# Optimization experiments

Hardware: AMD Instinct MI355X
Metric: run time of the kernel (lower is better)

The kernel has to match this reference:

```python
import jax, jax.numpy as jnp
import numpy as np

B = 16384          # batch
NS = 26            # sparse features
ND = 13            # dense features
V = 100000         # vocab per sparse feature
E = 16             # embedding size
H = 400            # dnn hidden
DNN_IN = NS * E + ND  # 429


def setup_inputs() -> dict:
    key = jax.random.key(0)
    ks = jax.random.split(key, 12)
    X_sparse = jax.random.randint(ks[0], (B, NS), 0, V, dtype=jnp.int32)
    X_dense = jax.random.normal(ks[1], (B, ND), dtype=jnp.float32)
    # stacked per-feature embedding tables: [NS, V, dim]
    emb1 = jax.random.normal(ks[2], (NS, V, 1), dtype=jnp.float32) * 1e-4
    emb2 = jax.random.normal(ks[3], (NS, V, E), dtype=jnp.float32) * 1e-4
    lin_weight = jax.random.normal(ks[4], (ND, 1), dtype=jnp.float32) * 1e-4
    bias = jnp.zeros((1,), dtype=jnp.float32)
    W0 = jax.random.normal(ks[5], (DNN_IN, H), dtype=jnp.float32) * 1e-4
    b0 = jnp.zeros((H,), dtype=jnp.float32)
    W1 = jax.random.normal(ks[6], (H, H), dtype=jnp.float32) * 1e-4
    b1 = jnp.zeros((H,), dtype=jnp.float32)
    W2 = jax.random.normal(ks[7], (H, H), dtype=jnp.float32) * 1e-4
    b2 = jnp.zeros((H,), dtype=jnp.float32)
    W_out = jax.random.normal(ks[8], (H, 1), dtype=jnp.float32) * 1e-4
    return {"X_sparse": X_sparse, "X_dense": X_dense, "emb1": emb1, "emb2": emb2,
            "lin_weight": lin_weight, "bias": bias, "W0": W0, "b0": b0,
            "W1": W1, "b1": b1, "W2": W2, "b2": b2, "W_out": W_out}


def reference(X_sparse, X_dense, emb1, emb2, lin_weight, bias, W0, b0, W1, b1, W2, b2, W_out):
    fidx = jnp.arange(NS)[None, :]            # [1, NS] feature indices
    # ---- FM linear term ----
    e1 = emb1[fidx, X_sparse][..., 0]          # [B, NS] per-feature scalar embeddings
    linear_sparse = jnp.sum(e1, axis=-1, keepdims=True)            # [B, 1]
    linear_dense = X_dense @ lin_weight                            # [B, 1]
    logit = linear_sparse + linear_dense
    # ---- FM second-order cross term ----
    e2 = emb2[fidx, X_sparse]                  # [B, NS, E]
    square_of_sum = jnp.square(jnp.sum(e2, axis=1))                # [B, E]
    sum_of_square = jnp.sum(jnp.square(e2), axis=1)                # [B, E]
    cross = 0.5 * jnp.sum(square_of_sum - sum_of_square, axis=-1, keepdims=True)
    logit = logit + cross
    # ---- DNN (dropout p=0 -> identity) ----
    dnn_in = jnp.concatenate([e2.reshape(e2.shape[0], -1), X_dense], axis=-1)  # [B, 429]
    h = jax.nn.relu(dnn_in @ W0 + b0)
    h = jax.nn.relu(h @ W1 + b1)
    h = jax.nn.relu(h @ W2 + b2)
    logit = logit + h @ W_out
    return logit + bias
```

## Files before the change

kernel.cpp:

```cpp
#include <hip/hip_runtime.h>
#include <hip/hip_bf16.h>

#define B_     16384
#define NS_    26
#define ND_    13
#define V_     100000
#define H_     400
#define NP     448
#define MT     64
#define ASTR   456
#define WCHB   (448 * 64)
#define WQTR   (112 * 64)

#define ACT_OFF   0
#define WBUF_OFF  (MT * ASTR)
#define FMV_OFF   (WBUF_OFF + 2 * WCHB)
#define DOT_OFF   (FMV_OFF + 256)
#define LDSB      (DOT_OFF + 256)

#define WAIT_VM7  0x0F77
#define WAIT_VM0  0x0F70

#define SC_A1   2097152.0f
#define SC_A2   2147483648.0f
#define SC_F0   0.125f
#define SC_F1   0.25f
#define SC_G    1.1368683772161603e-13f

typedef float f32x4 __attribute__((ext_vector_type(4)));

__device__ __forceinline__ unsigned char f2fp8(float v) {
  int pk = __builtin_amdgcn_cvt_pk_fp8_f32(v, v, 0, false);
  return (unsigned char)(pk & 0xff);
}

__global__ __launch_bounds__(256) void prep_w(
    const float* __restrict__ W0, const float* __restrict__ W1,
    const float* __restrict__ W2, const float* __restrict__ b0,
    const float* __restrict__ b1, const float* __restrict__ b2,
    const float* __restrict__ Wout,
    unsigned char* __restrict__ W0t, unsigned char* __restrict__ W1t,
    unsigned char* __restrict__ W2t, float* __restrict__ b0p,
    float* __restrict__ b1p, float* __restrict__ b2p,
    float* __restrict__ woutp) {
  const int blk = blockIdx.x;
  const int tid = threadIdx.x;
  if (blk < 147) {
    const int layer = blk / 49;
    const int t = blk - layer * 49;
    const int k0 = (t / 7) * 64, n0 = (t - (t / 7) * 7) * 64;
    const float* W = (layer == 0) ? W0 : (layer == 1) ? W1 : W2;
    unsigned char* Wt = (layer == 0) ? W0t : (layer == 1) ? W1t : W2t;
    const int Kdim = (layer == 0) ? 429 : 400;
    __shared__ float tile[64][65];
#pragma unroll
    for (int p = 0; p < 16; ++p) {
      int kk = p * 4 + (tid >> 6);
      int k = k0 + kk;
      int n = n0 + (tid & 63);
      float v = (k < Kdim && n < H_) ? W[k * H_ + n] : 0.f;
      tile[kk][tid & 63] = v;
    }
    __syncthreads();
#pragma unroll
    for (int p = 0; p < 4; ++p) {
      int nn = p * 16 + (tid >> 4);
      int n = n0 + nn;
      int k4 = (tid & 15) * 4;
      float sc[4];
#pragma unroll
      for (int i = 0; i < 4; ++i) {
        int kabs = k0 + k4 + i;
        sc[i] = (layer == 0 && kabs >= 416) ? 262144.0f : 4096.0f;
      }
      float v0 = tile[k4 + 0][nn] * sc[0];
      float v1 = tile[k4 + 1][nn] * sc[1];
      float v2 = tile[k4 + 2][nn] * sc[2];
      float v3 = tile[k4 + 3][nn] * sc[3];
      int w = __builtin_amdgcn_cvt_pk_fp8_f32(v0, v1, 0, false);
      w = __builtin_amdgcn_cvt_pk_fp8_f32(v2, v3, w, true);
      *(unsigned int*)(Wt + (size_t)n * NP + k0 + k4) = (unsigned int)w;
    }
  } else {
    for (int it = 0; it < 7; ++it) {
      int j = it * 256 + tid;
      if (j < NP)              b0p[j]          = (j < H_) ? b0[j] * SC_A1 : 0.f;
      else if (j < 2 * NP)     b1p[j - NP]     = (j - NP < H_) ? b1[j - NP] * SC_A2 : 0.f;
      else if (j < 3 * NP)     b2p[j - 2*NP]   = (j - 2*NP < H_) ? b2[j - 2*NP] : 0.f;
      else if (j < 4 * NP)     woutp[j - 3*NP] = (j - 3*NP < H_) ? Wout[j - 3*NP] : 0.f;
    }
  }
}

__device__ __forceinline__ void stage_w_chunk(
    const unsigned char* __restrict__ Wt, int kt, unsigned char* wb,
    int wave, int lane) {
  const unsigned char* wrow = Wt + (size_t)(wave * 112) * NP + kt * 64;
  unsigned char* lbase = wb + wave * WQTR;
#pragma unroll
  for (int i = 0; i < 7; ++i) {
    int s = i * 64 + lane;
    int nl = s >> 2;
    int g = (s & 3) ^ ((nl >> 1) & 3);
    const unsigned char* gp = wrow + (size_t)nl * NP + g * 16;
    unsigned char* lp = lbase + (size_t)(i * 64) * 16;
    __builtin_amdgcn_global_load_lds(
        (const __attribute__((address_space(1))) unsigned int*)gp,
        (__attribute__((address_space(3))) unsigned int*)lp, 16, 0, 0);
  }
}

__global__ __launch_bounds__(256, 1) void fused_all(
    const int* __restrict__ Xs, const float* __restrict__ Xd,
    const float* __restrict__ emb1, const float* __restrict__ emb2,
    const float* __restrict__ linw, const float* __restrict__ bias,
    const unsigned char* __restrict__ W0t, const unsigned char* __restrict__ W1t,
    const unsigned char* __restrict__ W2t,
    const float* __restrict__ b0p, const float* __restrict__ b1p,
    const float* __restrict__ b2p, const float* __restrict__ woutp,
    float* __restrict__ out) {
  extern __shared__ char smem[];
  unsigned char* act  = (unsigned char*)(smem + ACT_OFF);
  unsigned char* wbuf = (unsigned char*)(smem + WBUF_OFF);
  float* fmv  = (float*)(smem + FMV_OFF);
  float* dotv = (float*)(smem + DOT_OFF);

  const int tid  = threadIdx.x;
  const int wave = tid >> 6;
  const int lane = tid & 63;
  const int quad = lane >> 4;
  const int l16  = lane & 15;
  const int r0   = blockIdx.x * MT;

  stage_w_chunk(W0t, 0, wbuf, wave, lane);

  {
    if (tid < 64) dotv[tid] = 0.f;
    const int r   = lane >> 2;
    const int t4  = lane & 3;
    const int row = wave * 16 + r;
    const int gr  = r0 + row;
    const int* xs = Xs + gr * NS_;

    f32x4 sum = {0.f, 0.f, 0.f, 0.f}, sq = {0.f, 0.f, 0.f, 0.f};
#pragma unroll
    for (int f = 0; f < NS_; ++f) {
      int idx = xs[f];
      f32x4 v = *(const f32x4*)(emb2 + ((size_t)f * V_ + idx) * 16 + t4 * 4);
      sum += v;
      sq  += v * v;
      int pk = __builtin_amdgcn_cvt_pk_fp8_f32(v[0] * 4096.f, v[1] * 4096.f, 0, false);
      pk = __builtin_amdgcn_cvt_pk_fp8_f32(v[2] * 4096.f, v[3] * 4096.f, pk, true);
      *(unsigned int*)(act + row * ASTR + f * 16 + t4 * 4) = (unsigned int)pk;
    }

    float lin = 0.f;
    for (int f = t4; f < NS_; f += 4)
      lin += emb1[(size_t)f * V_ + xs[f]];

    for (int e = 416 + t4; e < NP; e += 4) act[row * ASTR + e] = 0;
    for (int e = t4; e < ND_; e += 4) {
      float xd = Xd[gr * ND_ + e];
      lin += xd * linw[e];
      act[row * ASTR + 416 + e] = f2fp8(xd * 64.f);
    }

    f32x4 c4 = sum * sum - sq;
    float fm = 0.5f * (c4[0] + c4[1] + c4[2] + c4[3]) + lin;
    fm += __shfl_xor(fm, 1, 64);
    fm += __shfl_xor(fm, 2, 64);
    if (t4 == 0) fmv[row] = fm + bias[0];
  }

  __syncthreads();

  const unsigned char* Wl[3] = {W0t, W1t, W2t};

  for (int layer = 0; layer < 3; ++layer) {
    const unsigned char* Wt = Wl[layer];
    const unsigned char* wq = wbuf + wave * WQTR;
    f32x4 acc[4][7] = {};

    for (int kt = 0; kt < 7; ++kt) {
      if (kt < 6) {
        stage_w_chunk(Wt, kt + 1, wbuf + ((kt + 1) & 1) * WCHB, wave, lane);
        __builtin_amdgcn_s_waitcnt(WAIT_VM7);
      } else {
        __builtin_amdgcn_s_waitcnt(WAIT_VM0);
      }
      __builtin_amdgcn_sched_barrier(0);
      const unsigned char* wb = wq + (kt & 1) * WCHB;

#pragma unroll
      for (int h = 0; h < 2; ++h) {
        long long av[4];
#pragma unroll
        for (int mt = 0; mt < 4; ++mt)
          av[mt] = *(const long long*)(act + (mt * 16 + l16) * ASTR + kt * 64 + h * 32 + quad * 8);
#pragma unroll
        for (int nt = 0; nt < 7; ++nt) {
          int nl = nt * 16 + l16;
          int sw = (2 * h + (quad >> 1)) ^ ((nl >> 1) & 3);
          long long bv = *(const long long*)(wb + nl * 64 + sw * 16 + (quad & 1) * 8);
#pragma unroll
          for (int mt = 0; mt < 4; ++mt)
            acc[mt][nt] = __builtin_amdgcn_mfma_f32_16x16x32_fp8_fp8(av[mt], bv, acc[mt][nt], 0, 0, 0);
        }
      }
    }

    if (layer < 2) stage_w_chunk(Wl[layer + 1], 0, wbuf, wave, lane);

    __syncthreads();

    if (layer < 2) {
      const float fs = (layer == 0) ? SC_F0 : SC_F1;
      const float* bl = (layer == 0) ? b0p : b1p;
#pragma unroll
      for (int nt = 0; nt < 7; ++nt) {
        int col = wave * 112 + nt * 16 + l16;
        float bz = bl[col];
#pragma unroll
        for (int mt = 0; mt < 4; ++mt) {
#pragma unroll
          for (int r = 0; r < 4; ++r) {
            float v = acc[mt][nt][r] * fs + bz;
            v = v > 0.f ? v : 0.f;
            act[(mt * 16 + quad * 4 + r) * ASTR + col] = f2fp8(v);
          }
        }
      }
    } else {
      float wsum[4][4] = {};
#pragma unroll
      for (int nt = 0; nt < 7; ++nt) {
        int col = wave * 112 + nt * 16 + l16;
        float bz = b2p[col];
        float wv = woutp[col];
#pragma unroll
        for (int mt = 0; mt < 4; ++mt) {
#pragma unroll
          for (int r = 0; r < 4; ++r) {
            float v = acc[mt][nt][r] * SC_G + bz;
            v = v > 0.f ? v : 0.f;
            wsum[mt][r] += v * wv;
          }
        }
      }
#pragma unroll
      for (int mt = 0; mt < 4; ++mt) {
#pragma unroll
        for (int r = 0; r < 4; ++r) {
          float s = wsum[mt][r];
          s += __shfl_xor(s, 1, 64);
          s += __shfl_xor(s, 2, 64);
          s += __shfl_xor(s, 4, 64);
          s += __shfl_xor(s, 8, 64);
          if (l16 == 0) atomicAdd(&dotv[mt * 16 + quad * 4 + r], s);
        }
      }
    }
    __syncthreads();
  }

  if (tid < 64) out[r0 + tid] = fmv[tid] + dotv[tid];
}

extern "C" void kernel_launch(void* const* d_in, const int* in_sizes, int n_in,
                              void* d_out, int out_size, void* d_ws, size_t ws_size,
                              hipStream_t stream) {
  const int*   Xs   = (const int*)d_in[0];
  const float* Xd   = (const float*)d_in[1];
  const float* emb1 = (const float*)d_in[2];
  const float* emb2 = (const float*)d_in[3];
  const float* linw = (const float*)d_in[4];
  const float* bias = (const float*)d_in[5];
  const float* W0   = (const float*)d_in[6];
  const float* b0   = (const float*)d_in[7];
  const float* W1   = (const float*)d_in[8];
  const float* b1   = (const float*)d_in[9];
  const float* W2   = (const float*)d_in[10];
  const float* b2   = (const float*)d_in[11];
  const float* Wout = (const float*)d_in[12];
  float* out = (float*)d_out;

  char* ws = (char*)d_ws;
  const size_t WSZ = (size_t)NP * NP;
  unsigned char* W0t = (unsigned char*)(ws);
  unsigned char* W1t = (unsigned char*)(ws + WSZ);
  unsigned char* W2t = (unsigned char*)(ws + 2 * WSZ);
  float* b0p   = (float*)(ws + 3 * WSZ);
  float* b1p   = (float*)(ws + 3 * WSZ + 1792);
  float* b2p   = (float*)(ws + 3 * WSZ + 2 * 1792);
  float* woutp = (float*)(ws + 3 * WSZ + 3 * 1792);

  (void)hipFuncSetAttribute((const void*)fused_all,
                            hipFuncAttributeMaxDynamicSharedMemorySize, LDSB);

  prep_w<<<148, 256, 0, stream>>>(W0, W1, W2, b0, b1, b2, Wout,
                                  W0t, W1t, W2t, b0p, b1p, b2p, woutp);

  fused_all<<<B_ / MT, 256, LDSB, stream>>>(
      Xs, Xd, emb1, emb2, linw, bias, W0t, W1t, W2t,
      b0p, b1p, b2p, woutp, out);
}
```

Baseline: 274.3 us.

## Halve row tile to 32, run two blocks per CU, split gather across waves

Reduces the per-block row tile from 64 to 32, doubling the grid and allowing two resident blocks per CU via launch bounds, which improves latency hiding for the embedding gathers. The gather phase is restructured so two waves handle the emb2 gathers, with all 26 loads issued up front, while the other two waves handle the emb1 linear term and dense features. Linear sums go into a separate LDS array that is combined at output. The trade-off is that each weight chunk staged into LDS now feeds half as many MFMAs, doubling weight traffic per row, and the smaller register budget per block risks spills.

```diff
diff --git a/kernel.cpp b/kernel.cpp
--- a/kernel.cpp
+++ b/kernel.cpp
@@ -7,7 +7,7 @@
 #define V_     100000
 #define H_     400
 #define NP     448
-#define MT     64
+#define MT     32
 #define ASTR   456
 #define WCHB   (448 * 64)
 #define WQTR   (112 * 64)
@@ -15,8 +15,9 @@
 #define ACT_OFF   0
 #define WBUF_OFF  (MT * ASTR)
 #define FMV_OFF   (WBUF_OFF + 2 * WCHB)
-#define DOT_OFF   (FMV_OFF + 256)
-#define LDSB      (DOT_OFF + 256)
+#define LINV_OFF  (FMV_OFF + 128)
+#define DOT_OFF   (LINV_OFF + 128)
+#define LDSB      (DOT_OFF + 128)
 
 #define WAIT_VM7  0x0F77
 #define WAIT_VM0  0x0F70
@@ -110,7 +111,7 @@
   }
 }
 
-__global__ __launch_bounds__(256, 1) void fused_all(
+__global__ __launch_bounds__(256, 2) void fused_all(
     const int* __restrict__ Xs, const float* __restrict__ Xd,
     const float* __restrict__ emb1, const float* __restrict__ emb2,
     const float* __restrict__ linw, const float* __restrict__ bias,
@@ -123,6 +124,7 @@
   unsigned char* act  = (unsigned char*)(smem + ACT_OFF);
   unsigned char* wbuf = (unsigned char*)(smem + WBUF_OFF);
   float* fmv  = (float*)(smem + FMV_OFF);
+  float* linv = (float*)(smem + LINV_OFF);
   float* dotv = (float*)(smem + DOT_OFF);
 
   const int tid  = threadIdx.x;
@@ -134,42 +136,59 @@
 
   stage_w_chunk(W0t, 0, wbuf, wave, lane);
 
+  if (tid < MT) dotv[tid] = 0.f;
+
   {
-    if (tid < 64) dotv[tid] = 0.f;
     const int r   = lane >> 2;
     const int t4  = lane & 3;
-    const int row = wave * 16 + r;
-    const int gr  = r0 + row;
-    const int* xs = Xs + gr * NS_;
-
-    f32x4 sum = {0.f, 0.f, 0.f, 0.f}, sq = {0.f, 0.f, 0.f, 0.f};
-#pragma unroll
-    for (int f = 0; f < NS_; ++f) {
-      int idx = xs[f];
-      f32x4 v = *(const f32x4*)(emb2 + ((size_t)f * V_ + idx) * 16 + t4 * 4);
-      sum += v;
-      sq  += v * v;
-      int pk = __builtin_amdgcn_cvt_pk_fp8_f32(v[0] * 4096.f, v[1] * 4096.f, 0, false);
-      pk = __builtin_amdgcn_cvt_pk_fp8_f32(v[2] * 4096.f, v[3] * 4096.f, pk, true);
-      *(unsigned int*)(act + row * ASTR + f * 16 + t4 * 4) = (unsigned int)pk;
-    }
-
-    float lin = 0.f;
-    for (int f = t4; f < NS_; f += 4)
-      lin += emb1[(size_t)f * V_ + xs[f]];
-
-    for (int e = 416 + t4; e < NP; e += 4) act[row * ASTR + e] = 0;
-    for (int e = t4; e < ND_; e += 4) {
-      float xd = Xd[gr * ND_ + e];
-      lin += xd * linw[e];
-      act[row * ASTR + 416 + e] = f2fp8(xd * 64.f);
-    }
-
-    f32x4 c4 = sum * sum - sq;
-    float fm = 0.5f * (c4[0] + c4[1] + c4[2] + c4[3]) + lin;
-    fm += __shfl_xor(fm, 1, 64);
-    fm += __shfl_xor(fm, 2, 64);
-    if (t4 == 0) fmv[row] = fm + bias[0];
+    if (wave < 2) {
+      const int row = wave * 16 + r;
+      const int gr  = r0 + row;
+      const int* xs = Xs + gr * NS_;
+      int idx[NS_];
+#pragma unroll
+      for (int f = 0; f < NS_; ++f) idx[f] = xs[f];
+      f32x4 v[NS_];
+#pragma unroll
+      for (int f = 0; f < NS_; ++f)
+        v[f] = *(const f32x4*)(emb2 + ((size_t)f * V_ + idx[f]) * 16 + t4 * 4);
+      f32x4 sum = {0.f, 0.f, 0.f, 0.f}, sq = {0.f, 0.f, 0.f, 0.f};
+#pragma unroll
+      for (int f = 0; f < NS_; ++f) {
+        sum += v[f];
+        sq  += v[f] * v[f];
+        int pk = __builtin_amdgcn_cvt_pk_fp8_f32(v[f][0] * 4096.f, v[f][1] * 4096.f, 0, false);
+        pk = __builtin_amdgcn_cvt_pk_fp8_f32(v[f][2] * 4096.f, v[f][3] * 4096.f, pk, true);
+        *(unsigned int*)(act + row * ASTR + f * 16 + t4 * 4) = (unsigned int)pk;
+      }
+      f32x4 c4 = sum * sum - sq;
+      float fm = 0.5f * (c4[0] + c4[1] + c4[2] + c4[3]);
+      fm += __shfl_xor(fm, 1, 64);
+      fm += __shfl_xor(fm, 2, 64);
+      if (t4 == 0) fmv[row] = fm + bias[0];
+    } else {
+      const int row = (wave - 2) * 16 + r;
+      const int gr  = r0 + row;
+      const int* xs = Xs + gr * NS_;
+      const float* ap[7];
+      int cnt = 0;
+      for (int f = t4; f < NS_; f += 4) ap[cnt++] = emb1 + (size_t)f * V_ + xs[f];
+      float ev[7];
+#pragma unroll
+      for (int j = 0; j < 7; ++j) if (j < cnt) ev[j] = *ap[j];
+      float lin = 0.f;
+#pragma unroll
+      for (int j = 0; j < 7; ++j) if (j < cnt) lin += ev[j];
+      for (int e = 416 + t4; e < NP; e += 4) act[row * ASTR + e] = 0;
+      for (int e = t4; e < ND_; e += 4) {
+        float xd = Xd[gr * ND_ + e];
+        lin += xd * linw[e];
+        act[row * ASTR + 416 + e] = f2fp8(xd * 64.f);
+      }
+      lin += __shfl_xor(lin, 1, 64);
+      lin += __shfl_xor(lin, 2, 64);
+      if (t4 == 0) linv[row] = lin;
+    }
   }
 
   __syncthreads();
@@ -179,7 +198,7 @@
   for (int layer = 0; layer < 3; ++layer) {
     const unsigned char* Wt = Wl[layer];
     const unsigned char* wq = wbuf + wave * WQTR;
-    f32x4 acc[4][7] = {};
+    f32x4 acc[2][7] = {};
 
     for (int kt = 0; kt < 7; ++kt) {
       if (kt < 6) {
@@ -193,9 +212,9 @@
 
 #pragma unroll
       for (int h = 0; h < 2; ++h) {
-        long long av[4];
-#pragma unroll
-        for (int mt = 0; mt < 4; ++mt)
+        long long av[2];
+#pragma unroll
+        for (int mt = 0; mt < 2; ++mt)
           av[mt] = *(const long long*)(act + (mt * 16 + l16) * ASTR + kt * 64 + h * 32 + quad * 8);
 #pragma unroll
         for (int nt = 0; nt < 7; ++nt) {
@@ -203,7 +222,7 @@
           int sw = (2 * h + (quad >> 1)) ^ ((nl >> 1) & 3);
           long long bv = *(const long long*)(wb + nl * 64 + sw * 16 + (quad & 1) * 8);
 #pragma unroll
-          for (int mt = 0; mt < 4; ++mt)
+          for (int mt = 0; mt < 2; ++mt)
             acc[mt][nt] = __builtin_amdgcn_mfma_f32_16x16x32_fp8_fp8(av[mt], bv, acc[mt][nt], 0, 0, 0);
         }
       }
@@ -221,7 +240,7 @@
         int col = wave * 112 + nt * 16 + l16;
         float bz = bl[col];
 #pragma unroll
-        for (int mt = 0; mt < 4; ++mt) {
+        for (int mt = 0; mt < 2; ++mt) {
 #pragma unroll
           for (int r = 0; r < 4; ++r) {
             float v = acc[mt][nt][r] * fs + bz;
@@ -231,14 +250,14 @@
         }
       }
     } else {
-      float wsum[4][4] = {};
+      float wsum[2][4] = {};
 #pragma unroll
       for (int nt = 0; nt < 7; ++nt) {
         int col = wave * 112 + nt * 16 + l16;
         float bz = b2p[col];
         float wv = woutp[col];
 #pragma unroll
-        for (int mt = 0; mt < 4; ++mt) {
+        for (int mt = 0; mt < 2; ++mt) {
 #pragma unroll
           for (int r = 0; r < 4; ++r) {
             float v = acc[mt][nt][r] * SC_G + bz;
@@ -248,7 +267,7 @@
         }
       }
 #pragma unroll
-      for (int mt = 0; mt < 4; ++mt) {
+      for (int mt = 0; mt < 2; ++mt) {
 #pragma unroll
         for (int r = 0; r < 4; ++r) {
           float s = wsum[mt][r];
@@ -263,7 +282,7 @@
     __syncthreads();
   }
 
-  if (tid < 64) out[r0 + tid] = fmv[tid] + dotv[tid];
+  if (tid < MT) out[r0 + tid] = fmv[tid] + linv[tid] + dotv[tid];
 }
 
 extern "C" void kernel_launch(void* const* d_in, const int* in_sizes, int n_in,
```

New measurement: 276.2 us. About the same (+0.7%).
